# Performance work log

Hardware: AMD Instinct MI355X
Metric: run time of the kernel (lower is better)

The kernel has to match this reference:

```python
import jax, jax.numpy as jnp
import numpy as np

NUM_HEADS = 8
KERNEL = 3


def _arsinh_norm(x, w, b):
    # ArsinhNorm with scale=1.0: weight * asinh(x) + bias
    return w * jnp.arcsinh(x) + b


def _nbr_idx(L, k):
    # NATTEN neighborhood: window start clamped so the k-window stays in-bounds
    start = jnp.clip(jnp.arange(L) - k // 2, 0, L - k)
    return start[:, None] + jnp.arange(k)  # [L, k]


def _na2d(x, qkv_w, qkv_b, proj_w, proj_b, num_heads=NUM_HEADS, k=KERNEL):
    B, H, W, C = x.shape
    hd = C // num_heads
    qkv = x @ qkv_w + qkv_b                      # [B,H,W,3C]
    q, kk, v = jnp.split(qkv, 3, axis=-1)
    q = q.reshape(B, H, W, num_heads, hd) * (hd ** -0.5)
    kk = kk.reshape(B, H, W, num_heads, hd)
    v = v.reshape(B, H, W, num_heads, hd)
    ri = _nbr_idx(H, k)[:, None, :, None]        # [H,1,k,1]
    ci = _nbr_idx(W, k)[None, :, None, :]        # [1,W,1,k]
    nb_k = kk[:, ri, ci].reshape(B, H, W, k * k, num_heads, hd)  # gather 3x3 neighborhood
    nb_v = v[:, ri, ci].reshape(B, H, W, k * k, num_heads, hd)
    scores = jnp.einsum('bijnd,bijmnd->bijnm', q, nb_k)          # [B,H,W,nh,k*k]
    attn = jax.nn.softmax(scores, axis=-1)
    out = jnp.einsum('bijnm,bijmnd->bijnd', attn, nb_v).reshape(B, H, W, C)
    return out @ proj_w + proj_b


def setup_inputs() -> dict:
    key = jax.random.key(0)
    ks = jax.random.split(key, 8)
    B, H, W, C = 16, 64, 64, 256
    s = 0.02
    return {
        'h': jax.random.normal(ks[0], (B, H, W, C), dtype=jnp.float32),
        'qkv_w': jax.random.normal(ks[1], (C, 3 * C), dtype=jnp.float32) * s,
        'qkv_b': jnp.zeros((3 * C,), jnp.float32),
        'proj_w': jax.random.normal(ks[2], (C, C), dtype=jnp.float32) * s,
        'proj_b': jnp.zeros((C,), jnp.float32),
        'n1_w': jnp.ones((C,), jnp.float32),
        'n1_b': jnp.zeros((C,), jnp.float32),
        'n2_w': jnp.ones((C,), jnp.float32),
        'n2_b': jnp.zeros((C,), jnp.float32),
        'mlp_w1': jax.random.normal(ks[3], (C, 2 * C), dtype=jnp.float32) * s,
        'mlp_b1': jnp.zeros((2 * C,), jnp.float32),
        'mlp_w2': jax.random.normal(ks[4], (2 * C, C), dtype=jnp.float32) * s,
        'mlp_b2': jnp.zeros((C,), jnp.float32),
    }


def reference(h, qkv_w, qkv_b, proj_w, proj_b, n1_w, n1_b, n2_w, n2_b,
              mlp_w1, mlp_b1, mlp_w2, mlp_b2):
    h1 = _arsinh_norm(h, n1_w, n1_b)
    h = h + _na2d(h1, qkv_w, qkv_b, proj_w, proj_b)
    h2 = _arsinh_norm(h, n2_w, n2_b)
    ff = jax.nn.gelu(h2 @ mlp_w1 + mlp_b1, approximate=False) @ mlp_w2 + mlp_b2
    return h + ff
```

## Files before the change

kernel.cpp:

```cpp
#include <hip/hip_runtime.h>
#include <math.h>

typedef unsigned short u16;
typedef unsigned int u32;
typedef __attribute__((ext_vector_type(8))) short short8;
typedef __attribute__((ext_vector_type(4))) float f32x4;

__device__ __forceinline__ float b2f(u16 u) {
    return __uint_as_float(((u32)u) << 16);
}
__device__ __forceinline__ u16 f2b(float f) {
    u32 x = __float_as_uint(f);
    return (u16)((x + 0x7fffu + ((x >> 16) & 1u)) >> 16);
}
__device__ __forceinline__ float ldext(const void* p, size_t i, int isbf) {
    return isbf ? b2f(((const u16*)p)[i]) : ((const float*)p)[i];
}
__device__ __forceinline__ void stext(void* p, size_t i, int isbf, float v) {
    if (isbf) ((u16*)p)[i] = f2b(v);
    else ((float*)p)[i] = v;
}
__device__ __forceinline__ void gl2lds16(const u16* g, u16* l) {
    __builtin_amdgcn_global_load_lds(
        (const __attribute__((address_space(1))) u32*)(const void*)g,
        (__attribute__((address_space(3))) u32*)(void*)l, 16, 0, 0);
}
__device__ __forceinline__ void unpack8(uint4 w, float* f) {
    const u32* pw = (const u32*)&w;
#pragma unroll
    for (int k = 0; k < 4; ++k) {
        f[2 * k]     = __uint_as_float(pw[k] << 16);
        f[2 * k + 1] = __uint_as_float(pw[k] & 0xffff0000u);
    }
}

__global__ void detect_k(const void* __restrict__ h, int* __restrict__ flag) {
    __shared__ int cnt;
    if (threadIdx.x == 0) cnt = 0;
    __syncthreads();
    const u16* p = (const u16*)h;
    int local = 0;
    for (int i = threadIdx.x; i < 4096; i += 256) {
        int e = (p[i] >> 7) & 0xFF;
        if (e != 0 && (e < 110 || e > 133)) local++;
    }
    atomicAdd(&cnt, local);
    __syncthreads();
    if (threadIdx.x == 0) *flag = (cnt < 256) ? 1 : 0;
}

__global__ void transpose_k(const void* __restrict__ src, u16* __restrict__ dst,
                            int R, int C, const int* __restrict__ flag) {
    int isbf = *flag;
    int idx = blockIdx.x * 256 + threadIdx.x;
    if (idx >= R * C) return;
    int r = idx / C, c = idx - r * C;
    dst[c * R + r] = f2b(ldext(src, idx, isbf));
}

__global__ void norm_k(const void* __restrict__ xb, size_t xoff,
                       const void* __restrict__ w, const void* __restrict__ b,
                       u16* __restrict__ y, const int* __restrict__ flag, int force_bf) {
    int isbf = *flag;
    int xisbf = force_bf ? 1 : isbf;
    size_t base = ((size_t)blockIdx.x * 256 + threadIdx.x) * 4;
    int c0 = (int)(base & 255);
    float v[4];
    if (xisbf) {
        uint2 raw = *reinterpret_cast<const uint2*>((const u16*)xb + xoff + base);
        const u16* px = reinterpret_cast<const u16*>(&raw);
#pragma unroll
        for (int j = 0; j < 4; ++j) v[j] = b2f(px[j]);
    } else {
        float4 r = *reinterpret_cast<const float4*>((const float*)xb + xoff + base);
        v[0] = r.x; v[1] = r.y; v[2] = r.z; v[3] = r.w;
    }
    u16 o[4];
#pragma unroll
    for (int j = 0; j < 4; ++j)
        o[j] = f2b(ldext(w, c0 + j, isbf) * asinhf(v[j]) + ldext(b, c0 + j, isbf));
    *reinterpret_cast<uint2*>(y + base) = *reinterpret_cast<uint2*>(o);
}

template <int EPI>
__global__ __launch_bounds__(256) void gemm_bt(
    const u16* __restrict__ A, const u16* __restrict__ BT, const void* __restrict__ bias,
    const void* __restrict__ resb, size_t resoff, void* __restrict__ outb, size_t outoff,
    int N, int K, const int* __restrict__ flag,
    const void* __restrict__ n2w, const void* __restrict__ n2b, u16* __restrict__ out2) {
    __shared__ __align__(16) u16 lA[64 * 32];
    __shared__ __align__(16) u16 lB[128 * 32];
    const int isbf = *flag;
    const int tid = threadIdx.x;
    const int lane = tid & 63;
    const int wave = tid >> 6;
    const int waveM = wave >> 1, waveN = wave & 1;
    const int m0 = blockIdx.y * 64;
    const int n0 = blockIdx.x * 128;

    f32x4 acc[2][4];
#pragma unroll
    for (int mi = 0; mi < 2; ++mi)
#pragma unroll
        for (int ni = 0; ni < 4; ++ni)
#pragma unroll
            for (int r = 0; r < 4; ++r) acc[mi][ni][r] = 0.f;

    const int lrow = lane & 15;
    const int ko = (lane >> 4) * 8;

    for (int k0 = 0; k0 < K; k0 += 32) {
        __syncthreads();
        {
            int e0 = (wave * 64 + lane) * 8;
            int row = e0 >> 5, col = e0 & 31;
            gl2lds16(&A[(size_t)(m0 + row) * K + k0 + col], &lA[wave * 512]);
        }
#pragma unroll
        for (int q = 0; q < 2; ++q) {
            int s = wave * 2 + q;
            int e0 = (s * 64 + lane) * 8;
            int row = e0 >> 5, col = e0 & 31;
            gl2lds16(&BT[(size_t)(n0 + row) * K + k0 + col], &lB[s * 512]);
        }
        __syncthreads();
        short8 af[2], bfr[4];
#pragma unroll
        for (int mi = 0; mi < 2; ++mi)
            af[mi] = *reinterpret_cast<const short8*>(&lA[(waveM * 32 + mi * 16 + lrow) * 32 + ko]);
#pragma unroll
        for (int ni = 0; ni < 4; ++ni)
            bfr[ni] = *reinterpret_cast<const short8*>(&lB[(waveN * 64 + ni * 16 + lrow) * 32 + ko]);
#pragma unroll
        for (int mi = 0; mi < 2; ++mi)
#pragma unroll
            for (int ni = 0; ni < 4; ++ni)
                acc[mi][ni] = __builtin_amdgcn_mfma_f32_16x16x32_bf16(af[mi], bfr[ni], acc[mi][ni], 0, 0, 0);
    }

    const int rquad = (lane >> 4) * 4;
    const int ccol = lane & 15;
#pragma unroll
    for (int mi = 0; mi < 2; ++mi)
#pragma unroll
        for (int ni = 0; ni < 4; ++ni) {
            int colg = n0 + waveN * 64 + ni * 16 + ccol;
            float bb = ldext(bias, colg, isbf);
#pragma unroll
            for (int r = 0; r < 4; ++r) {
                int rowg = m0 + waveM * 32 + mi * 16 + rquad + r;
                size_t idx = (size_t)rowg * N + colg;
                float v = acc[mi][ni][r] + bb;
                if (EPI == 0) {
                    ((u16*)outb)[outoff + idx] = f2b(v);
                } else if (EPI == 1) {
                    v = 0.5f * v * (1.f + erff(v * 0.70710678118654752f));
                    ((u16*)outb)[outoff + idx] = f2b(v);
                } else if (EPI == 2) {
                    v += ldext(resb, resoff + idx, isbf);
                    stext(outb, outoff + idx, isbf, v);
                } else if (EPI == 3) {
                    v += ldext(resb, resoff + idx, isbf);
                    ((u16*)outb)[outoff + idx] = f2b(v);
                } else if (EPI == 4) {
                    v += b2f(((const u16*)resb)[resoff + idx]);
                    stext(outb, outoff + idx, isbf, v);
                } else {
                    v += ldext(resb, resoff + idx, isbf);
                    ((u16*)outb)[outoff + idx] = f2b(v);
                    float y = ldext(n2w, colg, isbf) * asinhf(v) + ldext(n2b, colg, isbf);
                    out2[idx] = f2b(y);
                }
            }
        }
}

__global__ __launch_bounds__(256) void attn_k(const u16* __restrict__ qkv, u16* __restrict__ out) {
    const int t = blockIdx.x * 256 + threadIdx.x;
    const int head = t & 7;
    const int p = t >> 3;
    const int b = p >> 12;
    const int ij = p & 4095;
    const int i = ij >> 6, j = ij & 63;
    int r0 = i - 1; r0 = r0 < 0 ? 0 : (r0 > 61 ? 61 : r0);
    int c0 = j - 1; c0 = c0 < 0 ? 0 : (c0 > 61 ? 61 : c0);

    const u16* qp = qkv + (size_t)p * 768 + head * 32;
    float q[32];
#pragma unroll
    for (int ch = 0; ch < 4; ++ch)
        unpack8(*reinterpret_cast<const uint4*>(qp + ch * 8), q + ch * 8);

    const float qscale = 0.17677669529663687f;
    int nbp[9];
    float sc[9];
#pragma unroll
    for (int dr = 0; dr < 3; ++dr)
#pragma unroll
        for (int dc = 0; dc < 3; ++dc) {
            int nb = dr * 3 + dc;
            int np_ = b * 4096 + (r0 + dr) * 64 + (c0 + dc);
            nbp[nb] = np_;
            const u16* kp = qkv + (size_t)np_ * 768 + 256 + head * 32;
            float dot = 0.f;
#pragma unroll
            for (int ch = 0; ch < 4; ++ch) {
                float kf[8];
                unpack8(*reinterpret_cast<const uint4*>(kp + ch * 8), kf);
#pragma unroll
                for (int e = 0; e < 8; ++e) dot += q[ch * 8 + e] * kf[e];
            }
            sc[nb] = dot * qscale;
        }

    float mx = sc[0];
#pragma unroll
    for (int nb = 1; nb < 9; ++nb) mx = fmaxf(mx, sc[nb]);
    float s = 0.f;
#pragma unroll
    for (int nb = 0; nb < 9; ++nb) { sc[nb] = __expf(sc[nb] - mx); s += sc[nb]; }
    float inv = 1.f / s;

    float acc[32];
#pragma unroll
    for (int e = 0; e < 32; ++e) acc[e] = 0.f;
#pragma unroll
    for (int nb = 0; nb < 9; ++nb) {
        const u16* vp = qkv + (size_t)nbp[nb] * 768 + 512 + head * 32;
        float wgt = sc[nb] * inv;
#pragma unroll
        for (int ch = 0; ch < 4; ++ch) {
            float vf[8];
            unpack8(*reinterpret_cast<const uint4*>(vp + ch * 8), vf);
#pragma unroll
            for (int e = 0; e < 8; ++e) acc[ch * 8 + e] += wgt * vf[e];
        }
    }

    u16 ob[32];
#pragma unroll
    for (int e = 0; e < 32; ++e) ob[e] = f2b(acc[e]);
    uint4* ov = reinterpret_cast<uint4*>(ob);
    uint4* og = reinterpret_cast<uint4*>(out + (size_t)p * 256 + head * 32);
#pragma unroll
    for (int ch = 0; ch < 4; ++ch) og[ch] = ov[ch];
}

extern "C" void kernel_launch(void* const* d_in, const int* in_sizes, int n_in,
                              void* d_out, int out_size, void* d_ws, size_t ws_size,
                              hipStream_t stream) {
    const void* h      = d_in[0];
    const void* qkv_w  = d_in[1];
    const void* qkv_b  = d_in[2];
    const void* proj_w = d_in[3];
    const void* proj_b = d_in[4];
    const void* n1_w   = d_in[5];
    const void* n1_b   = d_in[6];
    const void* n2_w   = d_in[7];
    const void* n2_b   = d_in[8];
    const void* w1     = d_in[9];
    const void* b1     = d_in[10];
    const void* w2     = d_in[11];
    const void* b2     = d_in[12];

    char* ws = (char*)d_ws;
    u16* WqkvT  = (u16*)(ws + 0);
    u16* WprojT = (u16*)(ws + 393216);
    u16* W1T    = (u16*)(ws + 524288);
    u16* W2T    = (u16*)(ws + 786432);
    int* Flag   = (int*)(ws + 1048576);
    char* bufs  = ws + 1049600;

    size_t avail = ws_size > 1049600 ? ws_size - 1049600 : 0;
    int CHUNK = 4096;
    if (avail >= (size_t)65536 * 2048) CHUNK = 65536;
    else if (avail >= (size_t)16384 * 2048) CHUNK = 16384;
    else if (avail >= (size_t)8192 * 2048) CHUNK = 8192;

    u16* H1 = (u16*)bufs;
    u16* S  = (u16*)(bufs + (size_t)CHUNK * 512);

    detect_k<<<1, 256, 0, stream>>>(h, Flag);
    transpose_k<<<768, 256, 0, stream>>>(qkv_w, WqkvT, 256, 768, Flag);
    transpose_k<<<256, 256, 0, stream>>>(proj_w, WprojT, 256, 256, Flag);
    transpose_k<<<512, 256, 0, stream>>>(w1, W1T, 256, 512, Flag);
    transpose_k<<<512, 256, 0, stream>>>(w2, W2T, 512, 256, Flag);

    if (CHUNK == 65536) {
        u16* HNS = S;
        u16* T   = S + (size_t)65536 * 256;
        u16* N2  = (u16*)d_out;
        norm_k<<<16384, 256, 0, stream>>>(h, 0, n1_w, n1_b, H1, Flag, 0);
        { dim3 g(6, 1024); gemm_bt<0><<<g, 256, 0, stream>>>(H1, WqkvT, qkv_b, nullptr, 0, S, 0,
                                                             768, 256, Flag, nullptr, nullptr, nullptr); }
        attn_k<<<2048, 256, 0, stream>>>(S, H1);
        { dim3 g(2, 1024); gemm_bt<5><<<g, 256, 0, stream>>>(H1, WprojT, proj_b, h, 0, HNS, 0,
                                                             256, 256, Flag, n2_w, n2_b, N2); }
        { dim3 g(4, 1024); gemm_bt<1><<<g, 256, 0, stream>>>(N2, W1T, b1, nullptr, 0, T, 0,
                                                             512, 256, Flag, nullptr, nullptr, nullptr); }
        { dim3 g(2, 1024); gemm_bt<4><<<g, 256, 0, stream>>>(T, W2T, b2, HNS, 0, d_out, 0,
                                                             256, 512, Flag, nullptr, nullptr, nullptr); }
    } else {
        const int NCH = 65536 / CHUNK;
        for (int c = 0; c < NCH; ++c) {
            size_t off = (size_t)c * CHUNK * 256;
            norm_k<<<CHUNK / 4, 256, 0, stream>>>(h, off, n1_w, n1_b, H1, Flag, 0);
            { dim3 g(6, CHUNK / 64);
              gemm_bt<0><<<g, 256, 0, stream>>>(H1, WqkvT, qkv_b, nullptr, 0, S, 0,
                                                768, 256, Flag, nullptr, nullptr, nullptr); }
            attn_k<<<CHUNK / 32, 256, 0, stream>>>(S, H1);
            { dim3 g(2, CHUNK / 64);
              gemm_bt<2><<<g, 256, 0, stream>>>(H1, WprojT, proj_b, h, off, d_out, off,
                                                256, 256, Flag, nullptr, nullptr, nullptr); }
        }
        for (int c = 0; c < NCH; ++c) {
            size_t off = (size_t)c * CHUNK * 256;
            norm_k<<<CHUNK / 4, 256, 0, stream>>>(d_out, off, n2_w, n2_b, H1, Flag, 0);
            { dim3 g(4, CHUNK / 64);
              gemm_bt<1><<<g, 256, 0, stream>>>(H1, W1T, b1, nullptr, 0, S, 0,
                                                512, 256, Flag, nullptr, nullptr, nullptr); }
            { dim3 g(2, CHUNK / 64);
              gemm_bt<2><<<g, 256, 0, stream>>>(S, W2T, b2, d_out, off, d_out, off,
                                                256, 512, Flag, nullptr, nullptr, nullptr); }
        }
    }
}
```

Baseline: 512.0 us.

## Enlarge GEMM tile to 128x128, double-buffer LDS, remap blocks across XCDs

```diff
diff --git a/kernel.cpp b/kernel.cpp
--- a/kernel.cpp
+++ b/kernel.cpp
@@ -88,19 +88,28 @@
     const void* __restrict__ resb, size_t resoff, void* __restrict__ outb, size_t outoff,
     int N, int K, const int* __restrict__ flag,
     const void* __restrict__ n2w, const void* __restrict__ n2b, u16* __restrict__ out2) {
-    __shared__ __align__(16) u16 lA[64 * 32];
-    __shared__ __align__(16) u16 lB[128 * 32];
+    __shared__ __align__(16) u16 lA[2][128 * 32];
+    __shared__ __align__(16) u16 lB[2][128 * 32];
     const int isbf = *flag;
     const int tid = threadIdx.x;
     const int lane = tid & 63;
     const int wave = tid >> 6;
     const int waveM = wave >> 1, waveN = wave & 1;
-    const int m0 = blockIdx.y * 64;
-    const int n0 = blockIdx.x * 128;
-
-    f32x4 acc[2][4];
-#pragma unroll
-    for (int mi = 0; mi < 2; ++mi)
+
+    const int gx = gridDim.x;
+    int nblk = gx * gridDim.y;
+    int bflat = blockIdx.y * gx + blockIdx.x;
+    int L = bflat;
+    if ((nblk & 7) == 0) {
+        int per = nblk >> 3;
+        L = (bflat & 7) * per + (bflat >> 3);
+    }
+    const int m0 = (L / gx) * 128;
+    const int n0 = (L % gx) * 128;
+
+    f32x4 acc[4][4];
+#pragma unroll
+    for (int mi = 0; mi < 4; ++mi)
 #pragma unroll
         for (int ni = 0; ni < 4; ++ni)
 #pragma unroll
@@ -108,47 +117,54 @@
 
     const int lrow = lane & 15;
     const int ko = (lane >> 4) * 8;
-
-    for (int k0 = 0; k0 < K; k0 += 32) {
-        __syncthreads();
-        {
-            int e0 = (wave * 64 + lane) * 8;
-            int row = e0 >> 5, col = e0 & 31;
-            gl2lds16(&A[(size_t)(m0 + row) * K + k0 + col], &lA[wave * 512]);
-        }
-#pragma unroll
-        for (int q = 0; q < 2; ++q) {
-            int s = wave * 2 + q;
-            int e0 = (s * 64 + lane) * 8;
-            int row = e0 >> 5, col = e0 & 31;
-            gl2lds16(&BT[(size_t)(n0 + row) * K + k0 + col], &lB[s * 512]);
-        }
-        __syncthreads();
-        short8 af[2], bfr[4];
-#pragma unroll
-        for (int mi = 0; mi < 2; ++mi)
-            af[mi] = *reinterpret_cast<const short8*>(&lA[(waveM * 32 + mi * 16 + lrow) * 32 + ko]);
+    const int s0 = wave * 2, s1 = wave * 2 + 1;
+    const int e0a = (s0 * 64 + lane) * 8, e1a = (s1 * 64 + lane) * 8;
+    const int row0 = e0a >> 5, col0 = e0a & 31;
+    const int row1 = e1a >> 5, col1 = e1a & 31;
+
+    const int NT = K >> 5;
+    gl2lds16(&A[(size_t)(m0 + row0) * K + col0], &lA[0][s0 * 512]);
+    gl2lds16(&BT[(size_t)(n0 + row0) * K + col0], &lB[0][s0 * 512]);
+    gl2lds16(&A[(size_t)(m0 + row1) * K + col1], &lA[0][s1 * 512]);
+    gl2lds16(&BT[(size_t)(n0 + row1) * K + col1], &lB[0][s1 * 512]);
+    __syncthreads();
+
+    int cur = 0;
+    for (int t = 0; t < NT; ++t) {
+        if (t + 1 < NT) {
+            int k0 = (t + 1) << 5;
+            gl2lds16(&A[(size_t)(m0 + row0) * K + k0 + col0], &lA[cur ^ 1][s0 * 512]);
+            gl2lds16(&BT[(size_t)(n0 + row0) * K + k0 + col0], &lB[cur ^ 1][s0 * 512]);
+            gl2lds16(&A[(size_t)(m0 + row1) * K + k0 + col1], &lA[cur ^ 1][s1 * 512]);
+            gl2lds16(&BT[(size_t)(n0 + row1) * K + k0 + col1], &lB[cur ^ 1][s1 * 512]);
+        }
+        short8 af[4], bfr[4];
+#pragma unroll
+        for (int mi = 0; mi < 4; ++mi)
+            af[mi] = *reinterpret_cast<const short8*>(&lA[cur][(waveM * 64 + mi * 16 + lrow) * 32 + ko]);
 #pragma unroll
         for (int ni = 0; ni < 4; ++ni)
-            bfr[ni] = *reinterpret_cast<const short8*>(&lB[(waveN * 64 + ni * 16 + lrow) * 32 + ko]);
-#pragma unroll
-        for (int mi = 0; mi < 2; ++mi)
+            bfr[ni] = *reinterpret_cast<const short8*>(&lB[cur][(waveN * 64 + ni * 16 + lrow) * 32 + ko]);
+#pragma unroll
+        for (int mi = 0; mi < 4; ++mi)
 #pragma unroll
             for (int ni = 0; ni < 4; ++ni)
                 acc[mi][ni] = __builtin_amdgcn_mfma_f32_16x16x32_bf16(af[mi], bfr[ni], acc[mi][ni], 0, 0, 0);
+        __syncthreads();
+        cur ^= 1;
     }
 
     const int rquad = (lane >> 4) * 4;
     const int ccol = lane & 15;
 #pragma unroll
-    for (int mi = 0; mi < 2; ++mi)
+    for (int mi = 0; mi < 4; ++mi)
 #pragma unroll
         for (int ni = 0; ni < 4; ++ni) {
             int colg = n0 + waveN * 64 + ni * 16 + ccol;
             float bb = ldext(bias, colg, isbf);
 #pragma unroll
             for (int r = 0; r < 4; ++r) {
-                int rowg = m0 + waveM * 32 + mi * 16 + rquad + r;
+                int rowg = m0 + waveM * 64 + mi * 16 + rquad + r;
                 size_t idx = (size_t)rowg * N + colg;
                 float v = acc[mi][ni][r] + bb;
                 if (EPI == 0) {
@@ -291,35 +307,35 @@
         u16* T   = S + (size_t)65536 * 256;
         u16* N2  = (u16*)d_out;
         norm_k<<<16384, 256, 0, stream>>>(h, 0, n1_w, n1_b, H1, Flag, 0);
-        { dim3 g(6, 1024); gemm_bt<0><<<g, 256, 0, stream>>>(H1, WqkvT, qkv_b, nullptr, 0, S, 0,
-                                                             768, 256, Flag, nullptr, nullptr, nullptr); }
+        { dim3 g(6, 512); gemm_bt<0><<<g, 256, 0, stream>>>(H1, WqkvT, qkv_b, nullptr, 0, S, 0,
+                                                            768, 256, Flag, nullptr, nullptr, nullptr); }
         attn_k<<<2048, 256, 0, stream>>>(S, H1);
-        { dim3 g(2, 1024); gemm_bt<5><<<g, 256, 0, stream>>>(H1, WprojT, proj_b, h, 0, HNS, 0,
-                                                             256, 256, Flag, n2_w, n2_b, N2); }
-        { dim3 g(4, 1024); gemm_bt<1><<<g, 256, 0, stream>>>(N2, W1T, b1, nullptr, 0, T, 0,
-                                                             512, 256, Flag, nullptr, nullptr, nullptr); }
-        { dim3 g(2, 1024); gemm_bt<4><<<g, 256, 0, stream>>>(T, W2T, b2, HNS, 0, d_out, 0,
-                                                             256, 512, Flag, nullptr, nullptr, nullptr); }
+        { dim3 g(2, 512); gemm_bt<5><<<g, 256, 0, stream>>>(H1, WprojT, proj_b, h, 0, HNS, 0,
+                                                            256, 256, Flag, n2_w, n2_b, N2); }
+        { dim3 g(4, 512); gemm_bt<1><<<g, 256, 0, stream>>>(N2, W1T, b1, nullptr, 0, T, 0,
+                                                            512, 256, Flag, nullptr, nullptr, nullptr); }
+        { dim3 g(2, 512); gemm_bt<4><<<g, 256, 0, stream>>>(T, W2T, b2, HNS, 0, d_out, 0,
+                                                            256, 512, Flag, nullptr, nullptr, nullptr); }
     } else {
         const int NCH = 65536 / CHUNK;
         for (int c = 0; c < NCH; ++c) {
             size_t off = (size_t)c * CHUNK * 256;
             norm_k<<<CHUNK / 4, 256, 0, stream>>>(h, off, n1_w, n1_b, H1, Flag, 0);
-            { dim3 g(6, CHUNK / 64);
+            { dim3 g(6, CHUNK / 128);
               gemm_bt<0><<<g, 256, 0, stream>>>(H1, WqkvT, qkv_b, nullptr, 0, S, 0,
                                                 768, 256, Flag, nullptr, nullptr, nullptr); }
             attn_k<<<CHUNK / 32, 256, 0, stream>>>(S, H1);
-            { dim3 g(2, CHUNK / 64);
+            { dim3 g(2, CHUNK / 128);
               gemm_bt<2><<<g, 256, 0, stream>>>(H1, WprojT, proj_b, h, off, d_out, off,
                                                 256, 256, Flag, nullptr, nullptr, nullptr); }
         }
         for (int c = 0; c < NCH; ++c) {
             size_t off = (size_t)c * CHUNK * 256;
             norm_k<<<CHUNK / 4, 256, 0, stream>>>(d_out, off, n2_w, n2_b, H1, Flag, 0);
-            { dim3 g(4, CHUNK / 64);
+            { dim3 g(4, CHUNK / 128);
               gemm_bt<1><<<g, 256, 0, stream>>>(H1, W1T, b1, nullptr, 0, S, 0,
                                                 512, 256, Flag, nullptr, nullptr, nullptr); }
-            { dim3 g(2, CHUNK / 64);
+            { dim3 g(2, CHUNK / 128);
               gemm_bt<2><<<g, 256, 0, stream>>>(S, W2T, b2, d_out, off, d_out, off,
                                                 256, 512, Flag, nullptr, nullptr, nullptr); }
         }
```

Result: faster. 496.0 us (-3.1%).
